# Kernel tuning notes

Measured on AMD Instinct MI355X. Metric: run time of the kernel, lower is better.

## Reference

```python
import jax, jax.numpy as jnp
import numpy as np

# ---- static configuration (mirrors TimeFold init + deterministic prepare()) ----
B = 256
F = 512            # fft_length//2 + 1
T = 81             # input STFT frames
WIN = 1022         # window_length == frame_length == fft_length
HOP = 400          # hop_length
SEG = 1000         # segment_length
OVL = 50           # overlap_length
TO_HOP = 100       # deterministic choice of randint(1, hop_size=100)
SIG_LEN = (T - 1) * HOP + WIN            # 33022, inverse_stft output length

# prepare(): t segments kept, gaps of TO_HOP deleted
_t = SIG_LEN // (SEG + TO_HOP)
if SIG_LEN % (SEG + TO_HOP) >= SEG:
    _t += 1                               # _t = 30
KEPT_LEN = _t * SEG                       # 30000
OUT_LEN = SEG + (_t - 1) * (SEG - OVL)    # 28550
NF = 1 + (OUT_LEN - WIN) // HOP           # 69 output STFT frames

# indices kept after deleting the to_hop gaps (complement of delete_indices)
KEEP_IDX = np.concatenate([k * (SEG + TO_HOP) + np.arange(SEG) for k in range(_t)])

# overlap-add blending coefficients (length KEPT_LEN), built exactly as in prepare()
_ramp_up = np.arange(1, OVL + 1, dtype=np.float32) / OVL
_ramp_dn = np.arange(OVL, 0, -1, dtype=np.float32) / OVL
COEFF_INC = np.pad(np.tile(np.pad(_ramp_up, (0, SEG - OVL)), _t - 1), (SEG - OVL, OVL))
COEFF_DEC = np.pad(np.tile(np.pad(_ramp_dn, (SEG - OVL, 0)), _t - 1), (0, SEG))
_c = np.tile(np.pad(np.ones(SEG - 2 * OVL, np.float32), (OVL, OVL)), _t - 2)
_c = np.pad(np.pad(_c, (OVL, 0)), (SEG - OVL, 0), constant_values=1.0)
_c = np.pad(np.pad(_c, (0, OVL)), (0, SEG - OVL), constant_values=1.0)
COEFF_CONST = _c.astype(np.float32)

# final_delete_indices: drop [k*SEG, k*SEG+OVL) for k = 1.._t-1
_mask = np.ones(KEPT_LEN, bool)
for k in range(1, _t):
    _mask[k * SEG:k * SEG + OVL] = False
FINAL_KEEP = np.nonzero(_mask)[0]         # length OUT_LEN

# gather index grids for framing (static)
ISTFT_IDX = np.arange(T)[:, None] * HOP + np.arange(WIN)[None, :]
STFT_IDX = np.arange(NF)[:, None] * HOP + np.arange(WIN)[None, :]


def _hann(n):
    # periodic Hann, matches tf.signal.hann_window(periodic=True)
    return (0.5 - 0.5 * jnp.cos(2.0 * jnp.pi * jnp.arange(n, dtype=jnp.float32) / n)).astype(jnp.float32)


def _synthesis_window():
    w = _hann(WIN)
    denom = w * w
    overlaps = -(-WIN // HOP)
    denom = jnp.pad(denom, (0, overlaps * HOP - WIN))
    denom = denom.reshape(overlaps, HOP).sum(axis=0)
    denom = jnp.tile(denom, overlaps)[:WIN]
    return w / denom


def setup_inputs() -> dict:
    key = jax.random.key(0)
    x = jax.random.normal(key, (B, F, T, 2), dtype=jnp.float32)
    return {"x": x}


def reference(x) -> jnp.ndarray:
    # x: [B, 512, T, 2] real/imag STFT
    stfts = jax.lax.complex(x[..., 0], x[..., 1])          # [B, F, T]
    frames = jnp.transpose(stfts, (0, 2, 1))               # [B, T, F]
    # inverse_stft: irfft each frame, apply synthesis window, overlap-add
    tf_frames = jnp.fft.irfft(frames, n=WIN, axis=-1)
    tf_frames = tf_frames * _synthesis_window()
    sig = jnp.zeros((x.shape[0], SIG_LEN), jnp.float32).at[:, ISTFT_IDX].add(tf_frames)
    # dynamic segment delete (gather of kept indices)
    kept = sig[:, KEEP_IDX]                                # [B, KEPT_LEN]
    # shifted copy: drop first OVL samples, zero-pad at end
    shifted = jnp.concatenate(
        [kept[:, OVL:], jnp.zeros((x.shape[0], OVL), jnp.float32)], axis=1)
    # weighted overlap-add blend
    out = (jnp.asarray(COEFF_CONST) + jnp.asarray(COEFF_DEC)) * kept \
        + jnp.asarray(COEFF_INC) * shifted
    out = out[:, FINAL_KEEP]                               # [B, OUT_LEN]
    # forward STFT (periodic Hann, no padding)
    fr = out[:, STFT_IDX] * _hann(WIN)
    S = jnp.fft.rfft(fr, n=WIN, axis=-1)                   # [B, NF, 512]
    S = jnp.transpose(S, (0, 2, 1))                        # [B, 512, NF]
    return jnp.stack([S.real, S.imag], axis=-1)            # [B, 512, NF, 2]
```

## Files before the change

kernel.cpp:

```cpp
#include <hip/hip_runtime.h>
#include <math.h>

typedef unsigned short u16;
typedef unsigned int u32;

#define B_   256
#define F_   512
#define T_   81
#define WIN_ 1022
#define HOP_ 400
#define NF_  69
#define OUT_LEN_ 28550
#define SEG_ 1000
#define OVL_ 50

#define MA_  20736
#define MB_  17664
#define K_   1024
#define NBLK0 324
#define NBLK1 276

#define BASA_B     0u
#define BASB_B     (BASA_B + 2097152u)
#define ABUF_B     (BASB_B + 2097152u)
#define TF_B       (ABUF_B + 42467328u)
#define OUTF_B     (TF_B + 42467328u)
#define OUTF_STRIDE_ 28672

typedef __attribute__((ext_vector_type(8))) short bf8_t;
typedef __attribute__((ext_vector_type(4))) float f4_t;
typedef const __attribute__((address_space(1))) void* as1cv;
typedef __attribute__((address_space(3))) void* as3v;

__device__ __forceinline__ float b2f(u16 v) {
  u32 u = ((u32)v) << 16; float f; __builtin_memcpy(&f, &u, 4); return f;
}
__device__ __forceinline__ u16 f2b(float f) {
  u32 u; __builtin_memcpy(&u, &f, 4);
  return (u16)((u + 0x7fffu + ((u >> 16) & 1u)) >> 16);
}

__global__ __launch_bounds__(256) void gen_basisA(u16* __restrict__ BA) {
  int n = blockIdx.x;
  const float twopi_N = 6.283185307179586f / (float)WIN_;
  float scale = 0.f;
  if (n < WIN_) {
    float w = 0.5f - 0.5f * cosf(twopi_N * (float)n);
    int j = n % HOP_;
    float a = 0.5f - 0.5f * cosf(twopi_N * (float)j);
    float b = 0.5f - 0.5f * cosf(twopi_N * (float)(j + 400));
    float d = a * a + b * b;
    if (j + 800 < WIN_) {
      float c2 = 0.5f - 0.5f * cosf(twopi_N * (float)(j + 800));
      d += c2 * c2;
    }
    scale = (w / d) * (1.0f / (float)WIN_);
  }
  for (int k = threadIdx.x; k < 512; k += 256) {
    int m = (k * n) % WIN_;
    float ang = twopi_N * (float)m;
    float s, c; __sincosf(ang, &s, &c);
    bool edge = (k == 0) || (k == 511);
    float ck = edge ? 1.f : 2.f;
    float re = scale * ck * c;
    float im = edge ? 0.f : -scale * ck * s;
    BA[(size_t)n * K_ + 2 * k]     = f2b(re);
    BA[(size_t)n * K_ + 2 * k + 1] = f2b(im);
  }
}

__global__ __launch_bounds__(256) void gen_basisB(u16* __restrict__ BB) {
  int k = blockIdx.x;
  const float twopi_N = 6.283185307179586f / (float)WIN_;
  for (int w = threadIdx.x; w < K_; w += 256) {
    float re = 0.f, im = 0.f;
    if (w < WIN_) {
      int m = (k * w) % WIN_;
      float ang = twopi_N * (float)m;
      float s, c; __sincosf(ang, &s, &c);
      float h = 0.5f - 0.5f * cosf(twopi_N * (float)w);
      re = h * c; im = -h * s;
    }
    BB[(size_t)(2 * k)     * K_ + w] = f2b(re);
    BB[(size_t)(2 * k + 1) * K_ + w] = f2b(im);
  }
}

__global__ __launch_bounds__(256) void prep1(const float* __restrict__ x,
                                             u16* __restrict__ Abuf) {
  __shared__ float2 tile[32][33];
  int k0 = blockIdx.x * 32, t0 = blockIdx.y * 32, b = blockIdx.z;
  int c = threadIdx.x & 31, rr = threadIdx.x >> 5;
  const float2* xp = (const float2*)x;
#pragma unroll
  for (int i = 0; i < 4; ++i) {
    int k = k0 + rr + 8 * i, t = t0 + c;
    float2 v = make_float2(0.f, 0.f);
    if (t < T_) v = xp[(size_t)(b * F_ + k) * T_ + t];
    tile[rr + 8 * i][c] = v;
  }
  __syncthreads();
#pragma unroll
  for (int i = 0; i < 4; ++i) {
    int t = t0 + rr + 8 * i, kc = c;
    if (t < T_) {
      float2 v = tile[kc][rr + 8 * i];
      u32 packed = (u32)f2b(v.x) | ((u32)f2b(v.y) << 16);
      *(u32*)&Abuf[(size_t)(b * T_ + t) * K_ + 2 * (k0 + kc)] = packed;
    }
  }
}

template <int EPI>
__global__ __launch_bounds__(512, 2) void gemm_bf16(const u16* __restrict__ A,
                                                    const u16* __restrict__ Bt,
                                                    void* __restrict__ Cout) {
  __shared__ u16 sAB[4][16384];
  const int tid = threadIdx.x;
  const int lane = tid & 63, wv = tid >> 6;
  const int wm = wv >> 2, wn = wv & 3;
  const int fr = lane & 15, fq = lane >> 4;

  const int nwg = (EPI == 0) ? NBLK0 : NBLK1;
  const int q = nwg >> 3, r = nwg & 7;
  int orig = blockIdx.x;
  int xcd = orig & 7, pos = orig >> 3;
  int wgid = (xcd < r ? xcd * (q + 1) : r * (q + 1) + (xcd - r) * q) + pos;
  const int mt = wgid >> 2, nt = wgid & 3;
  const int bm = mt * 256, bn = nt * 256;

  const u16 *pA0, *pA1;
  if (EPI == 0) {
    pA0 = A + (size_t)(bm + 16 * wv + fr) * K_ + fq * 8;
    pA1 = A + (size_t)(bm + 16 * (wv + 8) + fr) * K_ + fq * 8;
  } else {
    int m0 = bm + 16 * wv + fr;
    int b0 = m0 / NF_, f0 = m0 - b0 * NF_;
    pA0 = A + (size_t)b0 * OUTF_STRIDE_ + f0 * HOP_ + fq * 8;
    int m1 = m0 + 128;
    int b1 = m1 / NF_, f1 = m1 - b1 * NF_;
    pA1 = A + (size_t)b1 * OUTF_STRIDE_ + f1 * HOP_ + fq * 8;
  }
  const u16* pB0 = Bt + (size_t)(bn + 16 * wv + fr) * K_ + fq * 8;
  const u16* pB1 = Bt + (size_t)(bn + 16 * (wv + 8) + fr) * K_ + fq * 8;

  f4_t acc[8][4];
#pragma unroll
  for (int i = 0; i < 8; ++i)
#pragma unroll
    for (int j = 0; j < 4; ++j) acc[i][j] = (f4_t){0.f, 0.f, 0.f, 0.f};

  auto STAGE_A = [&](int t) {
    const int buf = t & 3;
    const int ko = t * 32;
    __builtin_amdgcn_global_load_lds((as1cv)(const void*)(pA0 + ko),
                                     (as3v)(&sAB[buf][(wv)     * 512]), 16, 0, 0);
    __builtin_amdgcn_global_load_lds((as1cv)(const void*)(pA1 + ko),
                                     (as3v)(&sAB[buf][(wv + 8) * 512]), 16, 0, 0);
  };
  auto STAGE_B = [&](int t) {
    const int buf = t & 3;
    const int ko = t * 32;
    __builtin_amdgcn_global_load_lds((as1cv)(const void*)(pB0 + ko),
                                     (as3v)(&sAB[buf][8192 + (wv)     * 512]), 16, 0, 0);
    __builtin_amdgcn_global_load_lds((as1cv)(const void*)(pB1 + ko),
                                     (as3v)(&sAB[buf][8192 + (wv + 8) * 512]), 16, 0, 0);
  };

  STAGE_A(0); STAGE_B(0);
  STAGE_A(1); STAGE_B(1);
  STAGE_A(2); STAGE_B(2);
  asm volatile("s_waitcnt vmcnt(8)" ::: "memory");
  __builtin_amdgcn_s_barrier();

#pragma unroll
  for (int t = 0; t < 32; ++t) {
    const int buf = t & 3;
    const u16* sA = &sAB[buf][0];
    const u16* sB = &sAB[buf][8192];
    bf8_t a[8], b[4];

#pragma unroll
    for (int i = 0; i < 8; ++i)
      a[i] = *(const bf8_t*)&sA[(wm * 8 + i) * 512 + lane * 8];
#pragma unroll
    for (int j = 0; j < 2; ++j)
      b[j] = *(const bf8_t*)&sB[(wn * 4 + j) * 512 + lane * 8];
    if (t + 3 < 32) STAGE_A(t + 3);
    __builtin_amdgcn_s_barrier();
    asm volatile("s_waitcnt lgkmcnt(0)" ::: "memory");
    __builtin_amdgcn_s_setprio(1);
#pragma unroll
    for (int i = 0; i < 8; ++i)
#pragma unroll
      for (int j = 0; j < 2; ++j)
        acc[i][j] = __builtin_amdgcn_mfma_f32_16x16x32_bf16(a[i], b[j], acc[i][j], 0, 0, 0);
    __builtin_amdgcn_s_setprio(0);
    __builtin_amdgcn_s_barrier();

#pragma unroll
    for (int j = 2; j < 4; ++j)
      b[j] = *(const bf8_t*)&sB[(wn * 4 + j) * 512 + lane * 8];
    if (t + 3 < 32) STAGE_B(t + 3);
    __builtin_amdgcn_s_barrier();
    asm volatile("s_waitcnt lgkmcnt(0)" ::: "memory");
    __builtin_amdgcn_s_setprio(1);
#pragma unroll
    for (int i = 0; i < 8; ++i)
#pragma unroll
      for (int j = 2; j < 4; ++j)
        acc[i][j] = __builtin_amdgcn_mfma_f32_16x16x32_bf16(a[i], b[j], acc[i][j], 0, 0, 0);
    __builtin_amdgcn_s_setprio(0);

    if (t < 29)       asm volatile("s_waitcnt vmcnt(8)" ::: "memory");
    else if (t == 29) asm volatile("s_waitcnt vmcnt(4)" ::: "memory");
    else if (t == 30) asm volatile("s_waitcnt vmcnt(0)" ::: "memory");
    if (t < 31) __builtin_amdgcn_s_barrier();
  }

  if (EPI == 0) {
    u16* C = (u16*)Cout;
#pragma unroll
    for (int i = 0; i < 8; ++i)
#pragma unroll
      for (int j = 0; j < 4; ++j) {
        int colg = bn + wn * 64 + 16 * j + fr;
#pragma unroll
        for (int rr = 0; rr < 4; ++rr) {
          int rowg = bm + wm * 128 + 16 * i + fq * 4 + rr;
          C[(size_t)rowg * K_ + colg] = f2b(acc[i][j][rr]);
        }
      }
  } else {
    float* out = (float*)Cout;
    float* ep = (float*)((char*)&sAB[0][0] + wv * 8192);
    for (int j = 0; j < 4; ++j) {
#pragma unroll
      for (int i = 0; i < 8; ++i)
#pragma unroll
        for (int rr = 0; rr < 4; ++rr)
          ep[(16 * i + fq * 4 + rr) * 16 + fr] = acc[i][j][rr];
      asm volatile("s_waitcnt lgkmcnt(0)" ::: "memory");
      int colbase = bn + wn * 64 + 16 * j;
#pragma unroll
      for (int rr = 0; rr < 2; ++rr) {
        int row = lane + rr * 64;
        int m = bm + wm * 128 + row;
        int bb = m / NF_, ff = m - bb * NF_;
#pragma unroll
        for (int a2 = 0; a2 < 8; ++a2) {
          int k = (colbase >> 1) + a2;
          float2 v = make_float2(ep[row * 16 + 2 * a2], ep[row * 16 + 2 * a2 + 1]);
          ((float2*)out)[((size_t)bb * F_ + k) * NF_ + ff] = v;
        }
      }
    }
  }
}

__device__ __forceinline__ float sigval(const u16* __restrict__ tfb, int i) {
  int t1 = i / HOP_; if (t1 > T_ - 1) t1 = T_ - 1;
  int t0 = (i >= WIN_) ? (i - (WIN_ - 1) + HOP_ - 1) / HOP_ : 0;
  float acc = 0.f;
  for (int t = t0; t <= t1; ++t)
    acc += b2f(tfb[(size_t)t * K_ + (i - t * HOP_)]);
  return acc;
}

__global__ __launch_bounds__(256) void k3_fold(const u16* __restrict__ tf,
                                               u16* __restrict__ outf) {
  int id = blockIdx.x * 256 + threadIdx.x;
  if (id >= B_ * OUT_LEN_) return;
  int b = id / OUT_LEN_;
  int p = id - b * OUT_LEN_;
  int s, r;
  if (p < SEG_) { s = 0; r = p; }
  else {
    int q = p - SEG_;
    s = q / (SEG_ - OVL_) + 1;
    r = OVL_ + (q - (s - 1) * (SEG_ - OVL_));
  }
  const u16* tfb = tf + (size_t)b * T_ * K_;
  float val;
  if (r >= SEG_ - OVL_ && s <= 28) {
    float dec = (float)(SEG_ - r) * (1.f / (float)OVL_);
    float inc = (float)(r - (SEG_ - OVL_ - 1)) * (1.f / (float)OVL_);
    float v1 = sigval(tfb, s * 1100 + r);
    float v2 = sigval(tfb, (s + 1) * 1100 + (r - (SEG_ - OVL_)));
    val = dec * v1 + inc * v2;
  } else {
    val = sigval(tfb, s * 1100 + r);
  }
  outf[(size_t)b * OUTF_STRIDE_ + p] = f2b(val);
}

extern "C" void kernel_launch(void* const* d_in, const int* in_sizes, int n_in,
                              void* d_out, int out_size, void* d_ws, size_t ws_size,
                              hipStream_t stream) {
  const float* x = (const float*)d_in[0];
  char* ws = (char*)d_ws;
  u16* BA   = (u16*)(ws + BASA_B);
  u16* BB   = (u16*)(ws + BASB_B);
  u16* Abuf = (u16*)(ws + ABUF_B);
  u16* TF   = (u16*)(ws + TF_B);
  u16* outf = (u16*)(ws + OUTF_B);

  hipLaunchKernelGGL(gen_basisA, dim3(1024), dim3(256), 0, stream, BA);
  hipLaunchKernelGGL(gen_basisB, dim3(512), dim3(256), 0, stream, BB);
  hipLaunchKernelGGL(prep1, dim3(16, 3, 256), dim3(256), 0, stream, x, Abuf);
  hipLaunchKernelGGL((gemm_bf16<0>), dim3(NBLK0), dim3(512), 0, stream,
                     Abuf, BA, (void*)TF);
  int n3 = B_ * OUT_LEN_;
  hipLaunchKernelGGL(k3_fold, dim3((n3 + 255) / 256), dim3(256), 0, stream, TF, outf);
  hipLaunchKernelGGL((gemm_bf16<1>), dim3(NBLK1), dim3(512), 0, stream,
                     outf, BB, (void*)d_out);
}
```

Measured before the change: 315.5 us.

## Load B operand directly to registers, halving LDS footprint in bf16 GEMM

Result: slower. 392.9 us (+24.6%).

```diff
diff --git a/kernel.cpp b/kernel.cpp
--- a/kernel.cpp
+++ b/kernel.cpp
@@ -115,7 +115,7 @@
 __global__ __launch_bounds__(512, 2) void gemm_bf16(const u16* __restrict__ A,
                                                     const u16* __restrict__ Bt,
                                                     void* __restrict__ Cout) {
-  __shared__ u16 sAB[4][16384];
+  __shared__ u16 sA4[4][8192];
   const int tid = threadIdx.x;
   const int lane = tid & 63, wv = tid >> 6;
   const int wm = wv >> 2, wn = wv & 3;
@@ -141,8 +141,10 @@
     int b1 = m1 / NF_, f1 = m1 - b1 * NF_;
     pA1 = A + (size_t)b1 * OUTF_STRIDE_ + f1 * HOP_ + fq * 8;
   }
-  const u16* pB0 = Bt + (size_t)(bn + 16 * wv + fr) * K_ + fq * 8;
-  const u16* pB1 = Bt + (size_t)(bn + 16 * (wv + 8) + fr) * K_ + fq * 8;
+  const u16* pB[4];
+#pragma unroll
+  for (int j = 0; j < 4; ++j)
+    pB[j] = Bt + (size_t)(bn + wn * 64 + j * 16 + fr) * K_ + fq * 8;
 
   f4_t acc[8][4];
 #pragma unroll
@@ -154,68 +156,46 @@
     const int buf = t & 3;
     const int ko = t * 32;
     __builtin_amdgcn_global_load_lds((as1cv)(const void*)(pA0 + ko),
-                                     (as3v)(&sAB[buf][(wv)     * 512]), 16, 0, 0);
+                                     (as3v)(&sA4[buf][(wv)     * 512]), 16, 0, 0);
     __builtin_amdgcn_global_load_lds((as1cv)(const void*)(pA1 + ko),
-                                     (as3v)(&sAB[buf][(wv + 8) * 512]), 16, 0, 0);
+                                     (as3v)(&sA4[buf][(wv + 8) * 512]), 16, 0, 0);
   };
-  auto STAGE_B = [&](int t) {
-    const int buf = t & 3;
-    const int ko = t * 32;
-    __builtin_amdgcn_global_load_lds((as1cv)(const void*)(pB0 + ko),
-                                     (as3v)(&sAB[buf][8192 + (wv)     * 512]), 16, 0, 0);
-    __builtin_amdgcn_global_load_lds((as1cv)(const void*)(pB1 + ko),
-                                     (as3v)(&sAB[buf][8192 + (wv + 8) * 512]), 16, 0, 0);
+
+  bf8_t bX[4], bY[4];
+
+#pragma unroll
+  for (int j = 0; j < 4; ++j) bX[j] = *(const bf8_t*)&pB[j][0];
+  STAGE_A(0); STAGE_A(1); STAGE_A(2);
+  asm volatile("s_waitcnt vmcnt(4)" ::: "memory");
+  __builtin_amdgcn_s_barrier();
+
+  auto STEP = [&](int t, bf8_t (&bc)[4], bf8_t (&bnx)[4]) {
+    const u16* sAc = &sA4[t & 3][0];
+    bf8_t a[8];
+#pragma unroll
+    for (int i = 0; i < 8; ++i)
+      a[i] = *(const bf8_t*)&sAc[(wm * 8 + i) * 512 + lane * 8];
+    if (t + 1 < 32) {
+#pragma unroll
+      for (int j = 0; j < 4; ++j)
+        bnx[j] = *(const bf8_t*)&pB[j][(t + 1) * 32];
+    }
+    if (t + 3 < 32) STAGE_A(t + 3);
+    __builtin_amdgcn_s_setprio(1);
+#pragma unroll
+    for (int i = 0; i < 8; ++i)
+#pragma unroll
+      for (int j = 0; j < 4; ++j)
+        acc[i][j] = __builtin_amdgcn_mfma_f32_16x16x32_bf16(a[i], bc[j], acc[i][j], 0, 0, 0);
+    __builtin_amdgcn_s_setprio(0);
+    if (t <= 28)      asm volatile("s_waitcnt vmcnt(2)" ::: "memory");
+    else if (t <= 30) asm volatile("s_waitcnt vmcnt(0)" ::: "memory");
+    if (t < 31) __builtin_amdgcn_s_barrier();
   };
 
-  STAGE_A(0); STAGE_B(0);
-  STAGE_A(1); STAGE_B(1);
-  STAGE_A(2); STAGE_B(2);
-  asm volatile("s_waitcnt vmcnt(8)" ::: "memory");
-  __builtin_amdgcn_s_barrier();
-
-#pragma unroll
-  for (int t = 0; t < 32; ++t) {
-    const int buf = t & 3;
-    const u16* sA = &sAB[buf][0];
-    const u16* sB = &sAB[buf][8192];
-    bf8_t a[8], b[4];
-
-#pragma unroll
-    for (int i = 0; i < 8; ++i)
-      a[i] = *(const bf8_t*)&sA[(wm * 8 + i) * 512 + lane * 8];
-#pragma unroll
-    for (int j = 0; j < 2; ++j)
-      b[j] = *(const bf8_t*)&sB[(wn * 4 + j) * 512 + lane * 8];
-    if (t + 3 < 32) STAGE_A(t + 3);
-    __builtin_amdgcn_s_barrier();
-    asm volatile("s_waitcnt lgkmcnt(0)" ::: "memory");
-    __builtin_amdgcn_s_setprio(1);
-#pragma unroll
-    for (int i = 0; i < 8; ++i)
-#pragma unroll
-      for (int j = 0; j < 2; ++j)
-        acc[i][j] = __builtin_amdgcn_mfma_f32_16x16x32_bf16(a[i], b[j], acc[i][j], 0, 0, 0);
-    __builtin_amdgcn_s_setprio(0);
-    __builtin_amdgcn_s_barrier();
-
-#pragma unroll
-    for (int j = 2; j < 4; ++j)
-      b[j] = *(const bf8_t*)&sB[(wn * 4 + j) * 512 + lane * 8];
-    if (t + 3 < 32) STAGE_B(t + 3);
-    __builtin_amdgcn_s_barrier();
-    asm volatile("s_waitcnt lgkmcnt(0)" ::: "memory");
-    __builtin_amdgcn_s_setprio(1);
-#pragma unroll
-    for (int i = 0; i < 8; ++i)
-#pragma unroll
-      for (int j = 2; j < 4; ++j)
-        acc[i][j] = __builtin_amdgcn_mfma_f32_16x16x32_bf16(a[i], b[j], acc[i][j], 0, 0, 0);
-    __builtin_amdgcn_s_setprio(0);
-
-    if (t < 29)       asm volatile("s_waitcnt vmcnt(8)" ::: "memory");
-    else if (t == 29) asm volatile("s_waitcnt vmcnt(4)" ::: "memory");
-    else if (t == 30) asm volatile("s_waitcnt vmcnt(0)" ::: "memory");
-    if (t < 31) __builtin_amdgcn_s_barrier();
+  for (int tt = 0; tt < 16; ++tt) {
+    STEP(2 * tt,     bX, bY);
+    STEP(2 * tt + 1, bY, bX);
   }
 
   if (EPI == 0) {
@@ -226,33 +206,33 @@
       for (int j = 0; j < 4; ++j) {
         int colg = bn + wn * 64 + 16 * j + fr;
 #pragma unroll
-        for (int rr = 0; rr < 4; ++rr) {
-          int rowg = bm + wm * 128 + 16 * i + fq * 4 + rr;
-          C[(size_t)rowg * K_ + colg] = f2b(acc[i][j][rr]);
+        for (int rr2 = 0; rr2 < 4; ++rr2) {
+          int rowg = bm + wm * 128 + 16 * i + fq * 4 + rr2;
+          C[(size_t)rowg * K_ + colg] = f2b(acc[i][j][rr2]);
         }
       }
   } else {
+    __builtin_amdgcn_s_barrier();
     float* out = (float*)Cout;
-    float* ep = (float*)((char*)&sAB[0][0] + wv * 8192);
+    float* ep = (float*)&sA4[0][0] + (size_t)wv * 1088;
     for (int j = 0; j < 4; ++j) {
-#pragma unroll
-      for (int i = 0; i < 8; ++i)
-#pragma unroll
-        for (int rr = 0; rr < 4; ++rr)
-          ep[(16 * i + fq * 4 + rr) * 16 + fr] = acc[i][j][rr];
-      asm volatile("s_waitcnt lgkmcnt(0)" ::: "memory");
-      int colbase = bn + wn * 64 + 16 * j;
-#pragma unroll
-      for (int rr = 0; rr < 2; ++rr) {
-        int row = lane + rr * 64;
-        int m = bm + wm * 128 + row;
+      for (int rh = 0; rh < 2; ++rh) {
+#pragma unroll
+        for (int i2 = 0; i2 < 4; ++i2)
+#pragma unroll
+          for (int rr2 = 0; rr2 < 4; ++rr2)
+            ep[(16 * i2 + fq * 4 + rr2) * 17 + fr] = acc[rh * 4 + i2][j][rr2];
+        asm volatile("s_waitcnt lgkmcnt(0)" ::: "memory");
+        int m = bm + wm * 128 + rh * 64 + lane;
         int bb = m / NF_, ff = m - bb * NF_;
+        int colbase = bn + wn * 64 + 16 * j;
 #pragma unroll
         for (int a2 = 0; a2 < 8; ++a2) {
           int k = (colbase >> 1) + a2;
-          float2 v = make_float2(ep[row * 16 + 2 * a2], ep[row * 16 + 2 * a2 + 1]);
+          float2 v = make_float2(ep[lane * 17 + 2 * a2], ep[lane * 17 + 2 * a2 + 1]);
           ((float2*)out)[((size_t)bb * F_ + k) * NF_ + ff] = v;
         }
+        asm volatile("s_waitcnt lgkmcnt(0)" ::: "memory");
       }
     }
   }
```
